# Optimization experiments

Measured on AMD Instinct MI355X. Metric: run time of the kernel, lower is better.

## Reference

```python
import jax, jax.numpy as jnp
import numpy as np

MARGIN = 0.2
EPS = 1e-12  # F.normalize eps


def _l2norm(x, axis):
    n = jnp.linalg.norm(x, axis=axis, keepdims=True)
    return x / jnp.maximum(n, EPS)


def setup_inputs() -> dict:
    key = jax.random.key(0)
    k1, k2, k3, k4 = jax.random.split(key, 4)
    B, L_im, L_s, D = 256, 37, 33, 1024
    im_set = jax.random.normal(k1, (B, L_im, D), dtype=jnp.float32)
    s_seq = jax.random.normal(k2, (B, L_s, D), dtype=jnp.float32)
    # realistic valid lengths (>= a few regions/words, <= max)
    im_len = jax.random.randint(k3, (B,), 10, L_im + 1, dtype=jnp.int32)
    s_len = jax.random.randint(k4, (B,), 8, L_s + 1, dtype=jnp.int32)
    return {"im_set": im_set, "s_seq": s_seq, "im_len": im_len, "s_len": s_len}


def _aggr_similarity(im_set, s_seq, im_len, s_len):
    # l2-normalize feature dim, then drop CLS region / special tokens
    im = _l2norm(im_set, axis=2)[:, 1:, :]          # [B, Li, D]
    s = _l2norm(s_seq, axis=2)[:, 1:-2, :]          # [B, Ls, D]
    im_l = im_len - 1
    s_l = s_len - 3
    Li, Ls = im.shape[1], s.shape[1]
    # cross-batch alignment scores: [B_im, B_s, Li, Ls]
    align = jnp.einsum('bid,cjd->bcij', im, s)
    im_invalid = jnp.arange(Li)[None, :] >= im_l[:, None]   # [B, Li]
    s_invalid = jnp.arange(Ls)[None, :] >= s_l[:, None]     # [B, Ls]
    mask = im_invalid[:, None, :, None] | s_invalid[None, :, None, :]
    align = jnp.where(mask, 0.0, align)
    # 'MrSw': max over image regions, sum over sentence words
    return align.max(axis=2).sum(axis=2)             # [B_im, B_s]


def _contrastive_loss(scores):
    B = scores.shape[0]
    diag = jnp.diagonal(scores)                      # [B]
    cost_s = jnp.maximum(MARGIN + scores - diag[:, None], 0.0)
    cost_im = jnp.maximum(MARGIN + scores - diag[None, :], 0.0)
    eye = jnp.eye(B, dtype=bool)
    cost_s = jnp.where(eye, 0.0, cost_s)
    cost_im = jnp.where(eye, 0.0, cost_im)
    # max_violation=True: hardest negatives
    return cost_s.max(axis=1).sum() + cost_im.max(axis=0).sum()


def reference(im_set, s_seq, im_len, s_len):
    scores = _aggr_similarity(im_set, s_seq, im_len, s_len)
    return _contrastive_loss(scores)
```

## Files before the change

kernel.cpp:

```cpp
#include <hip/hip_runtime.h>
#include <hip/hip_bf16.h>


typedef __attribute__((ext_vector_type(8))) short bf16x8;
typedef __attribute__((ext_vector_type(4))) float f32x4;

#define NB   256
#define DIM  1024
#define LI   36
#define LS   30
#define MT   9
#define NT   15

static __device__ inline ushort f2bf(float x) {
    union { __hip_bfloat16 h; ushort u; } cvt;
    cvt.h = __float2bfloat16(x);
    return cvt.u;
}

static __device__ __forceinline__ void gload_lds16(const void* g, void* l) {
    __builtin_amdgcn_global_load_lds(
        (const __attribute__((address_space(1))) void*)g,
        (__attribute__((address_space(3))) void*)l, 16, 0, 0);
}

__global__ __launch_bounds__(256) void normalize_pack(
    const float* __restrict__ im, const float* __restrict__ sq,
    short* __restrict__ imp, short* __restrict__ sp)
{
    const int gw   = (blockIdx.x * 256 + threadIdx.x) >> 6;
    const int lane = threadIdx.x & 63;
    const int NIM  = NB * LI;

    const float* src;
    short* dst;
    if (gw < NIM) {
        int b = gw / LI, i = gw - b * LI;
        dst = imp + (size_t)gw * DIM;
        src = im + ((size_t)b * 37 + i + 1) * DIM;
    } else {
        int g2 = gw - NIM;
        int b = g2 / LS, j = g2 - b * LS;
        dst = sp + (size_t)g2 * DIM;
        src = sq + ((size_t)b * 33 + j + 1) * DIM;
    }

    const float4* s4 = (const float4*)src;
    float4 v[4];
    float ss = 0.f;
    #pragma unroll
    for (int t = 0; t < 4; ++t) {
        float4 x = s4[lane + 64 * t];
        v[t] = x;
        ss += x.x * x.x + x.y * x.y + x.z * x.z + x.w * x.w;
    }
    #pragma unroll
    for (int o = 32; o >= 1; o >>= 1) ss += __shfl_xor(ss, o, 64);
    float scale = 1.0f / fmaxf(sqrtf(ss), 1e-12f);
    ushort4* d4 = (ushort4*)dst;
    #pragma unroll
    for (int t = 0; t < 4; ++t) {
        float4 x = v[t];
        ushort4 o;
        o.x = f2bf(x.x * scale);
        o.y = f2bf(x.y * scale);
        o.z = f2bf(x.z * scale);
        o.w = f2bf(x.w * scale);
        d4[lane + 64 * t] = o;
    }
}

__global__ __launch_bounds__(512, 4) void gemm_scores(
    const short* __restrict__ imp, const short* __restrict__ sp,
    const int* __restrict__ im_len, const int* __restrict__ s_len,
    float* __restrict__ scores)
{
    __shared__ short As[144 * 64];
    __shared__ short Bs[240 * 64];
    __shared__ float sred[8][4][2];

    const int tid  = threadIdx.x;
    const int wave = tid >> 6;
    const int lane = tid & 63;
    const int q    = lane >> 4;
    const int l15  = lane & 15;
    const int b0   = blockIdx.x * 4;
    const int c0   = blockIdx.y * 8;

    const int nt0 = 2 * wave;
    const int nt1 = 2 * wave + 1;

    f32x4 acc[MT][2];
    #pragma unroll
    for (int mt = 0; mt < MT; ++mt)
        #pragma unroll
        for (int t = 0; t < 2; ++t)
            acc[mt][t] = (f32x4){0.f, 0.f, 0.f, 0.f};

    const int srow   = lane >> 3;
    const int schunk = (lane & 7) ^ srow;
    const char* gA = (const char*)imp + (size_t)(b0 * LI) * (DIM * 2)
                     + srow * (DIM * 2) + schunk * 16;
    const char* gB = (const char*)sp + (size_t)(c0 * LS) * (DIM * 2)
                     + srow * (DIM * 2) + schunk * 16;

    const int cs0 = (q ^ (l15 & 7)) * 16;
    const int cs1 = ((4 + q) ^ (l15 & 7)) * 16;

    for (int k0 = 0; k0 < DIM; k0 += 64) {
        const int kb = k0 * 2;
        #pragma unroll
        for (int it = 0; it < 3; ++it) {
            const int cid = it * 8 + wave;
            if (cid < 18)
                gload_lds16(gA + cid * (8 * DIM * 2) + kb, (char*)As + cid * 1024);
        }
        #pragma unroll
        for (int it = 0; it < 4; ++it) {
            const int cid = it * 8 + wave;
            if (cid < 30)
                gload_lds16(gB + cid * (8 * DIM * 2) + kb, (char*)Bs + cid * 1024);
        }
        __syncthreads();
        #pragma unroll
        for (int g = 0; g < 2; ++g) {
            const int cs = g ? cs1 : cs0;
            bf16x8 b0f = *(const bf16x8*)((const char*)Bs + (nt0 * 16 + l15) * 128 + cs);
            bf16x8 b1f;
            if (nt1 < NT)
                b1f = *(const bf16x8*)((const char*)Bs + (nt1 * 16 + l15) * 128 + cs);
            #pragma unroll
            for (int mt = 0; mt < MT; ++mt) {
                bf16x8 af = *(const bf16x8*)((const char*)As + (mt * 16 + l15) * 128 + cs);
                acc[mt][0] = __builtin_amdgcn_mfma_f32_16x16x32_bf16(af, b0f, acc[mt][0], 0, 0, 0);
                if (nt1 < NT)
                    acc[mt][1] = __builtin_amdgcn_mfma_f32_16x16x32_bf16(af, b1f, acc[mt][1], 0, 0, 0);
            }
        }
        __syncthreads();
    }

    int il[4];
    #pragma unroll
    for (int bb = 0; bb < 4; ++bb) il[bb] = im_len[b0 + bb] - 1;

    const int sbase = (32 * wave) / 30;
    float part[4][2] = {{0.f, 0.f}, {0.f, 0.f}, {0.f, 0.f}, {0.f, 0.f}};

    #pragma unroll
    for (int t = 0; t < 2; ++t) {
        const int nt = 2 * wave + t;
        if (nt >= NT) continue;
        const int col  = nt * 16 + l15;
        const int sidx = col / 30;
        const int j    = col - 30 * sidx;
        const int sl   = s_len[c0 + sidx] - 3;
        const bool jv  = (j < sl);
        const int s_begin = (nt * 16) / 30;
        const int s_end   = (nt * 16 + 15) / 30;

        #pragma unroll
        for (int bb = 0; bb < 4; ++bb) {
            const int ilb = il[bb];
            float m = -3.4e38f;
            #pragma unroll
            for (int mt = 0; mt < MT; ++mt) {
                const int im_lo = (4 * mt) / 9;
                const int im_hi = (4 * mt + 3) / 9;
                const int thr   = 9 * im_hi - 4 * mt;
                #pragma unroll
                for (int r = 0; r < 4; ++r) {
                    const float v = acc[mt][t][r];
                    const int base = mt * 16 + q * 4 + r;
                    if (im_lo == im_hi) {
                        if (im_lo == bb) {
                            const int i = base - 36 * bb;
                            if (i < ilb) m = fmaxf(m, v);
                        }
                    } else {
                        const bool hi = (q >= thr);
                        if (!hi && im_lo == bb) {
                            const int i = base - 36 * bb;
                            if (i < ilb) m = fmaxf(m, v);
                        } else if (hi && im_hi == bb) {
                            const int i = base - 36 * bb;
                            if (i < ilb) m = fmaxf(m, v);
                        }
                    }
                }
            }
            m = fmaxf(m, __shfl_xor(m, 16, 64));
            m = fmaxf(m, __shfl_xor(m, 32, 64));
            if (ilb < LI) m = fmaxf(m, 0.f);
            const float c = (q == 0 && jv) ? m : 0.f;
            #pragma unroll
            for (int slot = 0; slot < 2; ++slot) {
                const int s = sbase + slot;
                if (s >= s_begin && s <= s_end) {
                    float v = (sidx == s) ? c : 0.f;
                    #pragma unroll
                    for (int off = 32; off >= 1; off >>= 1) v += __shfl_xor(v, off, 64);
                    part[bb][slot] += v;
                }
            }
        }
    }

    if (lane == 0) {
        #pragma unroll
        for (int bb = 0; bb < 4; ++bb)
            #pragma unroll
            for (int slot = 0; slot < 2; ++slot)
                sred[wave][bb][slot] = part[bb][slot];
    }
    __syncthreads();
    if (tid < 32) {
        const int bb = tid >> 3, s = tid & 7;
        float v = 0.f;
        #pragma unroll
        for (int w = 0; w < 8; ++w) {
            const int slot = s - (32 * w) / 30;
            if (slot >= 0 && slot < 2) v += sred[w][bb][slot];
        }
        scores[(b0 + bb) * NB + c0 + s] = v;
    }
}

__global__ __launch_bounds__(256) void loss_partial(
    const float* __restrict__ sc, float* __restrict__ partial)
{
    const int wave = threadIdx.x >> 6, lane = threadIdx.x & 63;
    const int t = blockIdx.x * 4 + wave;
    const float dt = sc[t * (NB + 1)];
    float rowmax = 0.f, colmax = 0.f;
    #pragma unroll
    for (int p = 0; p < 4; ++p) {
        const int k = lane + 64 * p;
        const float r = sc[t * NB + k];
        const float c = sc[k * NB + t];
        if (k != t) {
            rowmax = fmaxf(rowmax, 0.2f + r - dt);
            colmax = fmaxf(colmax, 0.2f + c - dt);
        }
    }
    #pragma unroll
    for (int o = 32; o >= 1; o >>= 1) {
        rowmax = fmaxf(rowmax, __shfl_xor(rowmax, o, 64));
        colmax = fmaxf(colmax, __shfl_xor(colmax, o, 64));
    }
    if (lane == 0) partial[t] = fmaxf(rowmax, 0.f) + fmaxf(colmax, 0.f);
}

__global__ __launch_bounds__(256) void loss_final(
    const float* __restrict__ partial, float* __restrict__ out)
{
    const int t = threadIdx.x;
    float v = partial[t];
    __shared__ float red[4];
    #pragma unroll
    for (int o = 32; o >= 1; o >>= 1) v += __shfl_xor(v, o, 64);
    if ((t & 63) == 0) red[t >> 6] = v;
    __syncthreads();
    if (t == 0) out[0] = red[0] + red[1] + red[2] + red[3];
}

extern "C" void kernel_launch(void* const* d_in, const int* in_sizes, int n_in,
                              void* d_out, int out_size, void* d_ws, size_t ws_size,
                              hipStream_t stream) {
    const float* im_set = (const float*)d_in[0];
    const float* s_seq  = (const float*)d_in[1];
    const int*   im_len = (const int*)d_in[2];
    const int*   s_len  = (const int*)d_in[3];
    float* out = (float*)d_out;

    char* ws = (char*)d_ws;
    const size_t imp_bytes = (size_t)NB * LI * DIM * 2;
    const size_t sp_bytes  = (size_t)NB * LS * DIM * 2;
    short* imp    = (short*)ws;
    short* sp     = (short*)(ws + imp_bytes);
    float* scores = (float*)(ws + imp_bytes + sp_bytes);
    float* partial = (float*)(ws + imp_bytes + sp_bytes + (size_t)NB * NB * 4);

    normalize_pack<<<4224, 256, 0, stream>>>(im_set, s_seq, imp, sp);

    dim3 grid(NB / 4, NB / 8);
    gemm_scores<<<grid, 512, 0, stream>>>(imp, sp, im_len, s_len, scores);

    loss_partial<<<64, 256, 0, stream>>>(scores, partial);
    loss_final<<<1, 256, 0, stream>>>(partial, out);
}
```

Measured before the change: 260.6 us.

## Double-buffer LDS K-tiles and halve waves with 4 N-tiles each

Restructures the GEMM kernel to use 256 threads (4 waves), each computing 4 N-tiles instead of 2, with K-step 32 and a double-buffered LDS staging loop. The global->LDS loads for the next K-step are issued before computing the current one, which overlaps memory with MFMA and removes one barrier per step. It raises per-wave register use (36 accumulators) and lowers occupancy, and the last wave has only 3 valid tiles, so load imbalance grows.

```diff
diff --git a/kernel.cpp b/kernel.cpp
--- a/kernel.cpp
+++ b/kernel.cpp
@@ -11,6 +11,8 @@
 #define LS   30
 #define MT   9
 #define NT   15
+#define BUFB 24576
+#define BOFF 9216
 
 static __device__ inline ushort f2bf(float x) {
     union { __hip_bfloat16 h; ushort u; } cvt;
@@ -70,14 +72,13 @@
     }
 }
 
-__global__ __launch_bounds__(512, 4) void gemm_scores(
+__global__ __launch_bounds__(256, 3) void gemm_scores(
     const short* __restrict__ imp, const short* __restrict__ sp,
     const int* __restrict__ im_len, const int* __restrict__ s_len,
     float* __restrict__ scores)
 {
-    __shared__ short As[144 * 64];
-    __shared__ short Bs[240 * 64];
-    __shared__ float sred[8][4][2];
+    __shared__ __align__(1024) char lds[2 * BUFB];
+    __shared__ float sred[4][4][3];
 
     const int tid  = threadIdx.x;
     const int wave = tid >> 6;
@@ -87,69 +88,76 @@
     const int b0   = blockIdx.x * 4;
     const int c0   = blockIdx.y * 8;
 
-    const int nt0 = 2 * wave;
-    const int nt1 = 2 * wave + 1;
-
-    f32x4 acc[MT][2];
+    f32x4 acc[MT][4];
     #pragma unroll
     for (int mt = 0; mt < MT; ++mt)
         #pragma unroll
-        for (int t = 0; t < 2; ++t)
+        for (int t = 0; t < 4; ++t)
             acc[mt][t] = (f32x4){0.f, 0.f, 0.f, 0.f};
 
-    const int srow   = lane >> 3;
-    const int schunk = (lane & 7) ^ srow;
-    const char* gA = (const char*)imp + (size_t)(b0 * LI) * (DIM * 2)
-                     + srow * (DIM * 2) + schunk * 16;
-    const char* gB = (const char*)sp + (size_t)(c0 * LS) * (DIM * 2)
-                     + srow * (DIM * 2) + schunk * 16;
-
-    const int cs0 = (q ^ (l15 & 7)) * 16;
-    const int cs1 = ((4 + q) ^ (l15 & 7)) * 16;
-
-    for (int k0 = 0; k0 < DIM; k0 += 64) {
-        const int kb = k0 * 2;
-        #pragma unroll
-        for (int it = 0; it < 3; ++it) {
-            const int cid = it * 8 + wave;
-            if (cid < 18)
-                gload_lds16(gA + cid * (8 * DIM * 2) + kb, (char*)As + cid * 1024);
-        }
-        #pragma unroll
-        for (int it = 0; it < 4; ++it) {
-            const int cid = it * 8 + wave;
-            if (cid < 30)
-                gload_lds16(gB + cid * (8 * DIM * 2) + kb, (char*)Bs + cid * 1024);
+    const int r_in = lane >> 2;
+    const int sch  = (lane & 3) ^ (r_in & 3);
+    const char* gsrc[6];
+    int ldsoff[6];
+    #pragma unroll
+    for (int it = 0; it < 6; ++it) {
+        const int cid = wave * 6 + it;
+        ldsoff[it] = cid * 1024;
+        if (cid < 9)
+            gsrc[it] = (const char*)imp
+                + ((size_t)(b0 * LI) + cid * 16 + r_in) * (DIM * 2) + sch * 16;
+        else
+            gsrc[it] = (const char*)sp
+                + ((size_t)(c0 * LS) + (cid - 9) * 16 + r_in) * (DIM * 2) + sch * 16;
+    }
+
+    const int cs = (q ^ (l15 & 3)) * 16;
+
+    #pragma unroll
+    for (int it = 0; it < 6; ++it)
+        gload_lds16(gsrc[it], lds + ldsoff[it]);
+    __syncthreads();
+
+    auto kstep = [&](int curoff, int nxtoff, int kbn, bool do_stage) {
+        if (do_stage) {
+            #pragma unroll
+            for (int it = 0; it < 6; ++it)
+                gload_lds16(gsrc[it] + kbn, lds + nxtoff + ldsoff[it]);
+        }
+        bf16x8 bfr[4];
+        #pragma unroll
+        for (int t = 0; t < 4; ++t) {
+            const int nt = wave * 4 + t;
+            if (nt < NT)
+                bfr[t] = *(const bf16x8*)(lds + curoff + BOFF + (nt * 16 + l15) * 64 + cs);
+        }
+        #pragma unroll
+        for (int mt = 0; mt < MT; ++mt) {
+            bf16x8 af = *(const bf16x8*)(lds + curoff + (mt * 16 + l15) * 64 + cs);
+            #pragma unroll
+            for (int t = 0; t < 4; ++t)
+                if (wave * 4 + t < NT)
+                    acc[mt][t] = __builtin_amdgcn_mfma_f32_16x16x32_bf16(
+                        af, bfr[t], acc[mt][t], 0, 0, 0);
         }
         __syncthreads();
-        #pragma unroll
-        for (int g = 0; g < 2; ++g) {
-            const int cs = g ? cs1 : cs0;
-            bf16x8 b0f = *(const bf16x8*)((const char*)Bs + (nt0 * 16 + l15) * 128 + cs);
-            bf16x8 b1f;
-            if (nt1 < NT)
-                b1f = *(const bf16x8*)((const char*)Bs + (nt1 * 16 + l15) * 128 + cs);
-            #pragma unroll
-            for (int mt = 0; mt < MT; ++mt) {
-                bf16x8 af = *(const bf16x8*)((const char*)As + (mt * 16 + l15) * 128 + cs);
-                acc[mt][0] = __builtin_amdgcn_mfma_f32_16x16x32_bf16(af, b0f, acc[mt][0], 0, 0, 0);
-                if (nt1 < NT)
-                    acc[mt][1] = __builtin_amdgcn_mfma_f32_16x16x32_bf16(af, b1f, acc[mt][1], 0, 0, 0);
-            }
-        }
-        __syncthreads();
+    };
+
+    for (int kk = 0; kk < 16; ++kk) {
+        kstep(0, BUFB, (2 * kk + 1) * 64, true);
+        kstep(BUFB, 0, (2 * kk + 2) * 64, kk < 15);
     }
 
     int il[4];
     #pragma unroll
     for (int bb = 0; bb < 4; ++bb) il[bb] = im_len[b0 + bb] - 1;
 
-    const int sbase = (32 * wave) / 30;
-    float part[4][2] = {{0.f, 0.f}, {0.f, 0.f}, {0.f, 0.f}, {0.f, 0.f}};
-
-    #pragma unroll
-    for (int t = 0; t < 2; ++t) {
-        const int nt = 2 * wave + t;
+    const int sbase = (64 * wave) / 30;
+    float part[4][3] = {{0.f,0.f,0.f},{0.f,0.f,0.f},{0.f,0.f,0.f},{0.f,0.f,0.f}};
+
+    #pragma unroll
+    for (int t = 0; t < 4; ++t) {
+        const int nt = wave * 4 + t;
         if (nt >= NT) continue;
         const int col  = nt * 16 + l15;
         const int sidx = col / 30;
@@ -194,7 +202,7 @@
             if (ilb < LI) m = fmaxf(m, 0.f);
             const float c = (q == 0 && jv) ? m : 0.f;
             #pragma unroll
-            for (int slot = 0; slot < 2; ++slot) {
+            for (int slot = 0; slot < 3; ++slot) {
                 const int s = sbase + slot;
                 if (s >= s_begin && s <= s_end) {
                     float v = (sidx == s) ? c : 0.f;
@@ -210,7 +218,7 @@
         #pragma unroll
         for (int bb = 0; bb < 4; ++bb)
             #pragma unroll
-            for (int slot = 0; slot < 2; ++slot)
+            for (int slot = 0; slot < 3; ++slot)
                 sred[wave][bb][slot] = part[bb][slot];
     }
     __syncthreads();
@@ -218,9 +226,9 @@
         const int bb = tid >> 3, s = tid & 7;
         float v = 0.f;
         #pragma unroll
-        for (int w = 0; w < 8; ++w) {
-            const int slot = s - (32 * w) / 30;
-            if (slot >= 0 && slot < 2) v += sred[w][bb][slot];
+        for (int w = 0; w < 4; ++w) {
+            const int slot = s - (64 * w) / 30;
+            if (slot >= 0 && slot < 3) v += sred[w][bb][slot];
         }
         scores[(b0 + bb) * NB + c0 + s] = v;
     }
@@ -284,7 +292,7 @@
     normalize_pack<<<4224, 256, 0, stream>>>(im_set, s_seq, imp, sp);
 
     dim3 grid(NB / 4, NB / 8);
-    gemm_scores<<<grid, 512, 0, stream>>>(imp, sp, im_len, s_len, scores);
+    gemm_scores<<<grid, 256, 0, stream>>>(imp, sp, im_len, s_len, scores);
 
     loss_partial<<<64, 256, 0, stream>>>(scores, partial);
     loss_final<<<1, 256, 0, stream>>>(partial, out);
```

After: 750.8 us. 188% more time.
